# Kernel optimization log

Measured on AMD Instinct MI355X. Metric: run time of the kernel, lower is better.

## Reference

```python
import jax, jax.numpy as jnp
import numpy as np

LEAKY_SLOPE = 0.2
N_HEADS = 8
INPUT_DIM = 128
HEAD_DIM = 16  # embed_dim=128 // n_heads=8


def setup_inputs() -> dict:
    key = jax.random.key(0)
    k1, k2, k3, k4 = jax.random.split(key, 4)
    b, n = 4, 512
    h = jax.random.normal(k1, (b, n, INPUT_DIM), dtype=jnp.float32)
    mask = jnp.zeros((b, n, n), dtype=bool)  # 1 = attention not possible
    stdv_w = 1.0 / np.sqrt(HEAD_DIM)
    Wl = jax.random.uniform(k2, (N_HEADS, INPUT_DIM, HEAD_DIM), minval=-stdv_w, maxval=stdv_w, dtype=jnp.float32)
    Wr = jax.random.uniform(k3, (N_HEADS, INPUT_DIM, HEAD_DIM), minval=-stdv_w, maxval=stdv_w, dtype=jnp.float32)
    # Wak in torch is (n_heads, head_dim, 1); stdv = 1/sqrt(size(-1)) = 1
    Wak = jax.random.uniform(k4, (N_HEADS, HEAD_DIM), minval=-1.0, maxval=1.0, dtype=jnp.float32)
    return {"h": h, "mask": mask, "Wl": Wl, "Wr": Wr, "Wak": Wak}


def reference(h, mask, Wl, Wr, Wak):
    b, n, _ = h.shape
    # per-head projections: g = h @ W  -> (heads, batch, N, head_dim)
    g_l = jnp.einsum('bni,hid->hbnd', h, Wl)
    g_r = jnp.einsum('bni,hid->hbnd', h, Wr)
    # additive attention: LeakyReLU(g_l_i + g_r_j) . a  -> (heads, batch, N, N)
    e = jax.nn.leaky_relu(g_l[:, :, :, None, :] + g_r[:, :, None, :, :],
                          negative_slope=LEAKY_SLOPE)
    scores = jnp.einsum('hbijd,hd->hbij', e, Wak)
    scores = jnp.where(mask[None], -jnp.inf, scores)
    attn = jax.nn.softmax(scores, axis=-1)
    # weighted sum of g_r, then ReLU; output layout (batch, N, heads*head_dim)
    h_prime = jax.nn.relu(jnp.einsum('hbij,hbjd->bihd', attn, g_r))
    return h_prime.reshape(b, n, -1)
```

## Files before the change

### kernel.cpp

```cpp
#include <hip/hip_runtime.h>
#include <hip/hip_bf16.h>

#define B_SZ 4
#define N_SZ 512
#define IN_DIM 128
#define NH 8
#define HD 16
#define SLOPE 0.2f

#define ROWS 32
#define JT   16
#define TPB  512
#define GR_STRIDE 18
#define HROW (IN_DIM + 1)

typedef float v2f __attribute__((ext_vector_type(2)));

__device__ __forceinline__ v2f v2max(v2f a, v2f b) {
    v2f r; r.x = fmaxf(a.x, b.x); r.y = fmaxf(a.y, b.y); return r;
}


__global__ __launch_bounds__(256) void proj_kernel(
    const float* __restrict__ hin, const float* __restrict__ Wl,
    const float* __restrict__ Wr, float* __restrict__ gl, float* __restrict__ gr)
{
    int row = blockIdx.x;
    __shared__ float hrow[IN_DIM];
    int t = threadIdx.x;
    if (t < IN_DIM) hrow[t] = hin[(size_t)row * IN_DIM + t];
    __syncthreads();

    int side = t >> 7;
    int hd = t & 127;
    int head = hd >> 4, d = hd & 15;
    const float* W = (side ? Wr : Wl) + head * (IN_DIM * HD) + d;
    float acc = 0.f;
#pragma unroll 16
    for (int k = 0; k < IN_DIM; ++k)
        acc = fmaf(hrow[k], W[k * HD], acc);

    int b = row >> 9, i = row & (N_SZ - 1);
    float* g = side ? gr : gl;
    g[((size_t)(head * B_SZ + b) * N_SZ + i) * HD + d] = acc;
}

__global__ __launch_bounds__(TPB, 4) void attn_kernel(
    const float* __restrict__ gl, const float* __restrict__ gr,
    const float* __restrict__ Wak, const unsigned char* __restrict__ mask,
    float* __restrict__ out)
{
    __shared__ float grs[N_SZ * GR_STRIDE];
    __shared__ float gls[ROWS * HD];

    int bid = blockIdx.x;
    int itile = bid & 15;
    int hb = bid >> 4;
    int head = hb >> 2, b = hb & 3;
    int t = threadIdx.x;

    const float* grp = gr + (size_t)hb * (N_SZ * HD);
    for (int idx4 = t; idx4 < N_SZ * HD / 4; idx4 += TPB) {
        float4 v = ((const float4*)grp)[idx4];
        int j = idx4 >> 2, dq = (idx4 & 3) * 4;
        float* p = &grs[j * GR_STRIDE + dq];
        *(v2f*)p = (v2f){v.x, v.y};
        *(v2f*)(p + 2) = (v2f){v.z, v.w};
    }
    const float* glp = gl + ((size_t)hb * N_SZ + itile * ROWS) * HD;
    gls[t] = glp[t];
    __syncthreads();

    int il = t >> 4;
    int jt = t & 15;
    int i = itile * ROWS + il;

    v2f glv[HD / 2], av[HD / 2], o[HD / 2];
    const float* grow = &gls[il * HD];
#pragma unroll
    for (int e = 0; e < HD / 2; ++e) glv[e] = *(const v2f*)(grow + 2 * e);
    const float* ap = Wak + head * HD;
#pragma unroll
    for (int e = 0; e < HD / 2; ++e) av[e] = (v2f){ap[2 * e], ap[2 * e + 1]};
#pragma unroll
    for (int e = 0; e < HD / 2; ++e) o[e] = (v2f){0.f, 0.f};

    const unsigned char* mrow = mask + ((size_t)(b * N_SZ + i)) * N_SZ;
    const v2f slp = (v2f){SLOPE, SLOPE};
    float l = 0.f;

    for (int jj = 0; jj < N_SZ / JT; ++jj) {
        int j = jj * JT + jt;
        unsigned char mbit = mrow[j];
        const float* r = &grs[j * GR_STRIDE];
        v2f gj[HD / 2];
#pragma unroll
        for (int e = 0; e < HD / 2; ++e) gj[e] = *(const v2f*)(r + 2 * e);

        v2f sacc = (v2f){0.f, 0.f};
#pragma unroll
        for (int e = 0; e < HD / 2; ++e) {
            v2f x = glv[e] + gj[e];
            v2f lr = v2max(x, x * slp);
            sacc += av[e] * lr;
        }
        float s = sacc.x + sacc.y;
        s = fminf(s, 80.f);
        if (mbit) s = -1e30f;

        float p = __expf(s);
        l += p;
        v2f pv = (v2f){p, p};
#pragma unroll
        for (int e = 0; e < HD / 2; ++e)
            o[e] += pv * gj[e];
    }

#pragma unroll
    for (int off = 1; off < JT; off <<= 1) {
        l += __shfl_xor(l, off, 64);
#pragma unroll
        for (int e = 0; e < HD / 2; ++e) {
            v2f other;
            other.x = __shfl_xor(o[e].x, off, 64);
            other.y = __shfl_xor(o[e].y, off, 64);
            o[e] += other;
        }
    }

    if (jt == 0) {
        float inv = 1.f / l;
        float res[HD];
#pragma unroll
        for (int e = 0; e < HD / 2; ++e) {
            res[2 * e]     = fmaxf(o[e].x * inv, 0.f);
            res[2 * e + 1] = fmaxf(o[e].y * inv, 0.f);
        }
        float* op = out + ((size_t)(b * N_SZ + i)) * (NH * HD) + head * HD;
        *(float4*)op = *(float4*)res;
        *(float4*)(op + 4) = *(float4*)(res + 4);
        *(float4*)(op + 8) = *(float4*)(res + 8);
        *(float4*)(op + 12) = *(float4*)(res + 12);
    }
}


__global__ __launch_bounds__(TPB) void gatv2_fused(
    const float* __restrict__ hin, const unsigned char* __restrict__ mask,
    const float* __restrict__ Wl, const float* __restrict__ Wr,
    const float* __restrict__ Wak, float* __restrict__ out)
{
    __shared__ float wrs[IN_DIM * HD];
    __shared__ float hsh[ROWS][HROW];
    __shared__ float grs[N_SZ * GR_STRIDE];
    __shared__ float gls[ROWS][HD];

    int bid = blockIdx.x;
    int itile = bid & 15;
    int hb = bid >> 4;
    int head = hb >> 2, b = hb & 3;
    int t = threadIdx.x;

    int jl = t >> 4;
    int d  = t & 15;

    for (int idx = t; idx < IN_DIM * HD; idx += TPB)
        wrs[idx] = Wr[head * IN_DIM * HD + idx];

    const float* hb_base = hin + (size_t)b * N_SZ * IN_DIM;
    const float* wlcol = Wl + head * IN_DIM * HD + d;

    for (int c = 0; c < N_SZ / ROWS; ++c) {
        __syncthreads();
        const float* hc = hb_base + (size_t)c * ROWS * IN_DIM;
        for (int idx = t; idx < ROWS * IN_DIM; idx += TPB)
            hsh[idx >> 7][idx & 127] = hc[idx];
        __syncthreads();

        float acc = 0.f;
#pragma unroll 16
        for (int k = 0; k < IN_DIM; ++k)
            acc = fmaf(hsh[jl][k], wrs[k * HD + d], acc);
        grs[(c * ROWS + jl) * GR_STRIDE + d] = acc;

        if (c == itile) {
            float accl = 0.f;
#pragma unroll 16
            for (int k = 0; k < IN_DIM; ++k)
                accl = fmaf(hsh[jl][k], wlcol[k * HD], accl);
            gls[jl][d] = accl;
        }
    }
    __syncthreads();

    int il = jl;
    int jt = d;
    int i = itile * ROWS + il;

    float glv[HD], avv[HD];
#pragma unroll
    for (int dd = 0; dd < HD; ++dd) glv[dd] = gls[il][dd];
    const float* ap = Wak + head * HD;
#pragma unroll
    for (int dd = 0; dd < HD; ++dd) avv[dd] = ap[dd];

    const unsigned char* mrow = mask + ((size_t)(b * N_SZ + i)) * N_SZ;

    float m = -1e30f, l = 0.f;
    float o[HD];
#pragma unroll
    for (int dd = 0; dd < HD; ++dd) o[dd] = 0.f;

    for (int jj = 0; jj < N_SZ / JT; ++jj) {
        int j = jj * JT + jt;
        const float* r = &grs[j * GR_STRIDE];
        float gj[HD];
#pragma unroll
        for (int e = 0; e < HD / 2; ++e) {
            float2 v = *(const float2*)(r + 2 * e);
            gj[2 * e] = v.x; gj[2 * e + 1] = v.y;
        }

        float s = 0.f;
#pragma unroll
        for (int dd = 0; dd < HD; ++dd) {
            float x = glv[dd] + gj[dd];
            float lr = fmaxf(x, SLOPE * x);
            s = fmaf(avv[dd], lr, s);
        }
        if (mrow[j]) s = -1e30f;

        float mn = fmaxf(m, s);
        float cc = __expf(m - mn);
        float p = __expf(s - mn);
        l = fmaf(l, cc, p);
#pragma unroll
        for (int dd = 0; dd < HD; ++dd)
            o[dd] = fmaf(o[dd], cc, p * gj[dd]);
        m = mn;
    }

#pragma unroll
    for (int off = 1; off < JT; off <<= 1) {
        float mo = __shfl_xor(m, off, 64);
        float lo = __shfl_xor(l, off, 64);
        float mn = fmaxf(m, mo);
        float c1 = __expf(m - mn), c2 = __expf(mo - mn);
        l = l * c1 + lo * c2;
#pragma unroll
        for (int dd = 0; dd < HD; ++dd)
            o[dd] = o[dd] * c1 + __shfl_xor(o[dd], off, 64) * c2;
        m = mn;
    }

    if (jt == 0) {
        float inv = 1.f / l;
        float res[HD];
#pragma unroll
        for (int dd = 0; dd < HD; ++dd)
            res[dd] = fmaxf(o[dd] * inv, 0.f);
        float* op = out + ((size_t)(b * N_SZ + i)) * (NH * HD) + head * HD;
#pragma unroll
        for (int e = 0; e < HD / 4; ++e)
            *(float4*)(op + 4 * e) = *(float4*)(res + 4 * e);
    }
}

extern "C" void kernel_launch(void* const* d_in, const int* in_sizes, int n_in,
                              void* d_out, int out_size, void* d_ws, size_t ws_size,
                              hipStream_t stream) {
    const float* hin = (const float*)d_in[0];
    const unsigned char* mask = (const unsigned char*)d_in[1];
    const float* Wl = (const float*)d_in[2];
    const float* Wr = (const float*)d_in[3];
    const float* Wak = (const float*)d_in[4];
    float* out = (float*)d_out;
    (void)in_sizes; (void)n_in; (void)out_size;

    const size_t g_elems = (size_t)NH * B_SZ * N_SZ * HD;
    const size_t need = 2 * g_elems * sizeof(float);

    if (ws_size >= need && d_ws != nullptr) {
        float* gl = (float*)d_ws;
        float* gr = gl + g_elems;
        proj_kernel<<<B_SZ * N_SZ, 256, 0, stream>>>(hin, Wl, Wr, gl, gr);
        attn_kernel<<<NH * B_SZ * (N_SZ / ROWS), TPB, 0, stream>>>(
            gl, gr, Wak, mask, out);
    } else {
        gatv2_fused<<<NH * B_SZ * (N_SZ / ROWS), TPB, 0, stream>>>(
            hin, mask, Wl, Wr, Wak, out);
    }
}
```

Baseline: 93.21 us.

## Rewrite LeakyReLU score as linear plus abs term with precomputed dot products

Uses the identity leaky(x)=0.6x+0.4|x| so the score splits into a precomputed a·gl term per row, a precomputed a·gr term per column stored in shared memory, and a sum of 0.4·a·|gl+gr|, swapping max/mul per element for abs modifiers. Mask bytes are also preloaded into a 32-bit register bitmask before the loop, and the main loop is unrolled by four. The cost is an extra shared array, an extra barrier and slightly different rounding.

```diff
diff --git a/kernel.cpp b/kernel.cpp
--- a/kernel.cpp
+++ b/kernel.cpp
@@ -15,10 +15,6 @@
 #define HROW (IN_DIM + 1)
 
 typedef float v2f __attribute__((ext_vector_type(2)));
-
-__device__ __forceinline__ v2f v2max(v2f a, v2f b) {
-    v2f r; r.x = fmaxf(a.x, b.x); r.y = fmaxf(a.y, b.y); return r;
-}
 
 
 __global__ __launch_bounds__(256) void proj_kernel(
@@ -52,6 +48,7 @@
 {
     __shared__ float grs[N_SZ * GR_STRIDE];
     __shared__ float gls[ROWS * HD];
+    __shared__ float crs[N_SZ];
 
     int bid = blockIdx.x;
     int itile = bid & 15;
@@ -71,42 +68,67 @@
     gls[t] = glp[t];
     __syncthreads();
 
+    const float* ap = Wak + head * HD;
+
+    {
+        const float* r = &grs[t * GR_STRIDE];
+        float acc = 0.f;
+#pragma unroll
+        for (int dd = 0; dd < HD; ++dd) acc = fmaf(ap[dd], r[dd], acc);
+        crs[t] = 0.6f * acc;
+    }
+    __syncthreads();
+
     int il = t >> 4;
     int jt = t & 15;
     int i = itile * ROWS + il;
 
-    v2f glv[HD / 2], av[HD / 2], o[HD / 2];
+    v2f glv[HD / 2], o[HD / 2];
+    float av04[HD];
     const float* grow = &gls[il * HD];
 #pragma unroll
     for (int e = 0; e < HD / 2; ++e) glv[e] = *(const v2f*)(grow + 2 * e);
-    const float* ap = Wak + head * HD;
-#pragma unroll
-    for (int e = 0; e < HD / 2; ++e) av[e] = (v2f){ap[2 * e], ap[2 * e + 1]};
+    float cl06;
+    {
+        float acc = 0.f;
+#pragma unroll
+        for (int dd = 0; dd < HD; ++dd) acc = fmaf(ap[dd], grow[dd], acc);
+        cl06 = 0.6f * acc;
+    }
+#pragma unroll
+    for (int dd = 0; dd < HD; ++dd) av04[dd] = 0.4f * ap[dd];
 #pragma unroll
     for (int e = 0; e < HD / 2; ++e) o[e] = (v2f){0.f, 0.f};
 
     const unsigned char* mrow = mask + ((size_t)(b * N_SZ + i)) * N_SZ;
-    const v2f slp = (v2f){SLOPE, SLOPE};
+    unsigned mbits = 0;
+#pragma unroll
+    for (int jj = 0; jj < N_SZ / JT; ++jj)
+        mbits |= (mrow[jj * JT + jt] ? 1u : 0u) << jj;
+
     float l = 0.f;
 
+#pragma unroll 4
     for (int jj = 0; jj < N_SZ / JT; ++jj) {
         int j = jj * JT + jt;
-        unsigned char mbit = mrow[j];
         const float* r = &grs[j * GR_STRIDE];
         v2f gj[HD / 2];
 #pragma unroll
         for (int e = 0; e < HD / 2; ++e) gj[e] = *(const v2f*)(r + 2 * e);
 
-        v2f sacc = (v2f){0.f, 0.f};
+        v2f xv[HD / 2];
+#pragma unroll
+        for (int e = 0; e < HD / 2; ++e) xv[e] = glv[e] + gj[e];
+
+        float s0 = cl06 + crs[j];
+        float s1 = 0.f;
 #pragma unroll
         for (int e = 0; e < HD / 2; ++e) {
-            v2f x = glv[e] + gj[e];
-            v2f lr = v2max(x, x * slp);
-            sacc += av[e] * lr;
-        }
-        float s = sacc.x + sacc.y;
-        s = fminf(s, 80.f);
-        if (mbit) s = -1e30f;
+            s0 = fmaf(av04[2 * e],     fabsf(xv[e].x), s0);
+            s1 = fmaf(av04[2 * e + 1], fabsf(xv[e].y), s1);
+        }
+        float s = fminf(s0 + s1, 80.f);
+        if (mbits & (1u << jj)) s = -1e30f;
 
         float p = __expf(s);
         l += p;
```

Measured after the change: 91.82 us. No clear change (-1.5%).
